# Optimization experiments

Measured on AMD Instinct MI355X. Metric: run time of the kernel, lower is better.

The kernel has to match this reference:

```python
import jax, jax.numpy as jnp
import numpy as np

NUM_HEADS = 4
D_K = 64
D_MODEL = NUM_HEADS * D_K  # 256
SEN_LEN = 8192
N_GROUPS = 4096
BASE_LEN = 64
N_EDGES = N_GROUPS * BASE_LEN  # 262144
PATH_LEN = 64


def setup_inputs() -> dict:
    rng = np.random.default_rng(0)
    key = jax.random.key(0)
    ks = jax.random.split(key, 16)

    # ragged group lengths, each >= 2, summing exactly to N_EDGES
    half = N_GROUPS // 2
    r = rng.integers(-(BASE_LEN - 2), BASE_LEN - 1, size=half)
    edge_len = np.concatenate([BASE_LEN + r, BASE_LEN - r]).astype(np.int64)
    assert edge_len.sum() == N_EDGES and edge_len.min() >= 2

    # distinct token ids; include src=0 and tar=1 so path_agg branches fire
    perm = rng.permutation(np.arange(2, SEN_LEN))[: N_GROUPS - 2]
    token_ids = np.concatenate([np.array([0, 1]), perm]).astype(np.int64)

    def w(k, shape):
        return jax.random.normal(k, shape, jnp.float32) / np.sqrt(shape[-1]).astype(np.float32)

    return {
        "path": jax.random.normal(ks[0], (PATH_LEN, D_MODEL), jnp.float32),
        "path_len": PATH_LEN,
        "q": jax.random.normal(ks[1], (SEN_LEN, D_MODEL), jnp.float32),
        "k": jax.random.normal(ks[2], (N_EDGES, D_MODEL), jnp.float32),
        "v": jax.random.normal(ks[3], (N_EDGES, D_MODEL), jnp.float32),
        "graphs": 0,
        "edge_len": jnp.asarray(edge_len),
        "token_ids": jnp.asarray(token_ids),
        "pair": jnp.array([0, 1], jnp.int32),
        "rev": 0,
        "W_qpair": w(ks[4], (D_MODEL, 2 * D_MODEL)),
        "W_pk": w(ks[5], (D_MODEL, D_MODEL)),
        "W_pv": w(ks[6], (D_MODEL, D_MODEL)),
        "W_q": w(ks[7], (D_MODEL, D_MODEL)),
        "W_k": w(ks[8], (D_MODEL, D_MODEL)),
        "W_v": w(ks[9], (D_MODEL, D_MODEL)),
        "W_out": w(ks[10], (D_MODEL, D_MODEL)),
        "b_out": jnp.zeros((D_MODEL,), jnp.float32),
        "W_agg": w(ks[11], (D_MODEL, 2 * D_MODEL)),
    }


def _forward(path, q, k, v, edge_len, token_ids, pair, rev,
             W_qpair, W_pk, W_pv, W_q, W_k, W_v, W_out, b_out, W_agg):
    H, dk = NUM_HEADS, D_K
    G = edge_len.shape[0]
    E = k.shape[0]
    scale = 1.0 / jnp.sqrt(jnp.float32(dk))

    src = pair[0] if rev == 0 else pair[1]
    tar = pair[1] if rev == 0 else pair[0]

    # pair query: cat(q[src], q[tar]) -> linear -> [H, 1, dk]
    pair_q = (jnp.concatenate([q[src], q[tar]]) @ W_qpair.T).reshape(1, H, dk).transpose(1, 0, 2)

    qh = (q @ W_q.T).reshape(-1, H, dk).transpose(1, 0, 2)      # [H, S, dk]
    pk = (path @ W_pk.T).reshape(-1, H, dk).transpose(1, 0, 2)  # [H, P, dk]
    pv = (path @ W_pv.T).reshape(-1, H, dk).transpose(1, 0, 2)  # [H, P, dk]
    kh = (k @ W_k.T).reshape(-1, H, dk).transpose(1, 0, 2)      # [H, E, dk]
    vh = (v @ W_v.T).reshape(-1, H, dk).transpose(1, 0, 2)      # [H, E, dk]

    # ---- pair/path attention ----
    att = jax.nn.softmax(jnp.einsum('hqd,hpd->hqp', pair_q, pk) * scale, axis=-1)  # [H,1,P]
    path_vals = jnp.einsum('hqp,hpd->hqd', att, pv).sum(axis=1)  # [H, dk]
    path_result = path_vals.reshape(-1) @ W_out.T + b_out        # [d_model]

    # ---- segmented per-group attention (vectorized ragged loop) ----
    seg = jnp.repeat(jnp.arange(G), edge_len, total_repeat_length=E)  # [E]
    q_sel = qh[:, token_ids, :]          # [H, G, dk] query per group
    qe = q_sel[:, seg, :]                # [H, E, dk] query per edge
    # torch.matmul(q_[H,dk], k_[H,i,dk].T) broadcasts to cross-head logits [a,b,i]
    logits = jnp.einsum('aed,bed->eab', qe, kh) * scale  # [E, H, H]
    lmax = jax.lax.stop_gradient(jax.ops.segment_max(logits, seg, num_segments=G))
    ex = jnp.exp(logits - lmax[seg])
    denom = jax.ops.segment_sum(ex, seg, num_segments=G)
    p = ex / denom[seg]                                   # segmented softmax [E, H, H]
    # sum over key-head b per edge, then segment-reduce over edges of each group
    out_e = jnp.einsum('eab,bed->ead', p, vh)             # [E, H, dk]
    hid = jax.ops.segment_sum(out_e, seg, num_segments=G) # [G, H, dk]
    new_hid = hid.reshape(G, H * dk) @ W_out.T + b_out    # [G, d_model] (dropout=identity)

    # ---- assemble output rows ----
    pr = jnp.broadcast_to(path_result, (G, D_MODEL))
    feat_path = jnp.concatenate([new_hid, pr], axis=1) @ W_agg.T  # token == src
    path_feat = jnp.concatenate([pr, new_hid], axis=1) @ W_agg.T  # token == tar
    is_src = (token_ids == src)[:, None]
    is_tar = (token_ids == tar)[:, None]
    vals = jnp.where(is_src, feat_path, jnp.where(is_tar, path_feat, new_hid))
    returned = q.at[token_ids].set(vals)
    return returned, att


def reference(path, path_len, q, k, v, graphs, edge_len, token_ids, pair, rev,
              W_qpair, W_pk, W_pv, W_q, W_k, W_v, W_out, b_out, W_agg):
    return _forward(path, q, k, v, edge_len, token_ids, pair, rev,
                    W_qpair, W_pk, W_pv, W_q, W_k, W_v, W_out, b_out, W_agg)
```

## Files before the change

### kernel.cpp

```cpp
#include <hip/hip_runtime.h>
#include <hip/hip_bf16.h>

#define H 4
#define DK 64
#define DM 256
#define SEN 8192
#define NG 4096
#define ETOT 262144
#define PLEN 64
#define MAXE 128

typedef unsigned short ushortT;
typedef __attribute__((ext_vector_type(8))) __bf16 bf16x8;
typedef __attribute__((ext_vector_type(8))) unsigned short us8;
typedef __attribute__((ext_vector_type(4))) unsigned short us4;
typedef __attribute__((ext_vector_type(4))) float f32x4;

#define TMS 264

__device__ __forceinline__ ushortT f2bf(float f) {
    unsigned u = __float_as_uint(f);
    u += 0x7FFF + ((u >> 16) & 1);
    return (ushortT)(u >> 16);
}
__device__ __forceinline__ bf16x8 ldb8(const ushortT* p) {
    us8 v = *(const us8*)p;
    return __builtin_bit_cast(bf16x8, v);
}
__device__ __forceinline__ bf16x8 pack8(const float* f) {
    us8 v;
#pragma unroll
    for (int j = 0; j < 8; j++) v[j] = f2bf(f[j]);
    return __builtin_bit_cast(bf16x8, v);
}
__device__ __forceinline__ ushortT sbf(float f) {
    return __builtin_bit_cast(ushortT, (__bf16)f);
}
__device__ __forceinline__ bf16x8 pack8f(float4 a, float4 b) {
    bf16x8 r;
    r[0] = (__bf16)a.x; r[1] = (__bf16)a.y; r[2] = (__bf16)a.z; r[3] = (__bf16)a.w;
    r[4] = (__bf16)b.x; r[5] = (__bf16)b.y; r[6] = (__bf16)b.z; r[7] = (__bf16)b.w;
    return r;
}

__global__ __launch_bounds__(256) void scan_kernel(const int* __restrict__ edge_len,
                                                   int* __restrict__ starts) {
    __shared__ int part[256];
    const int tid = threadIdx.x;
    const int base = tid * 16;
    int loc[16];
    int s = 0;
#pragma unroll
    for (int i = 0; i < 16; i++) { loc[i] = s; s += edge_len[base + i]; }
    part[tid] = s;
    __syncthreads();
    if (tid == 0) {
        int acc = 0;
        for (int i = 0; i < 256; i++) { int t = part[i]; part[i] = acc; acc += t; }
    }
    __syncthreads();
    const int off = part[tid];
#pragma unroll
    for (int i = 0; i < 16; i++) starts[base + i] = off + loc[i];
}

__global__ void copy_kernel(const float* __restrict__ q, float* __restrict__ out) {
    const size_t i = (size_t)blockIdx.x * blockDim.x + threadIdx.x;
    ((float4*)out)[i] = ((const float4*)q)[i];
}

__global__ __launch_bounds__(256) void wprep_kernel(
    const float* __restrict__ W_q, const float* __restrict__ W_k,
    const float* __restrict__ W_v, const float* __restrict__ W_out,
    ushortT* __restrict__ WQb, ushortT* __restrict__ WKTb,
    ushortT* __restrict__ WVb, ushortT* __restrict__ WOb) {
    const int idx = blockIdx.x * 256 + threadIdx.x;
    const int sel = idx >> 16;
    const int i = idx & 65535;
    if (sel == 0) {
        WQb[i] = sbf(W_q[i]);
    } else if (sel == 1) {
        const int c = i >> 8, d = i & 255;
        WKTb[i] = sbf(W_k[d * DM + c]);
    } else if (sel == 2) {
        WVb[i] = sbf(W_v[i]);
    } else {
        WOb[i] = sbf(W_out[i]);
    }
}

__global__ __launch_bounds__(256) void qhtmat_kernel(
    const float* __restrict__ q, const int* __restrict__ token_ids,
    const ushortT* __restrict__ WQb, const ushortT* __restrict__ WKTb,
    ushortT* __restrict__ tmat_u) {
    __shared__ ushortT Al[16 * 264];
    __shared__ ushortT QHs[16 * 264];
    const int tid = threadIdx.x;
    const int g0 = blockIdx.x * 16;
    const int lane = tid & 63, w = tid >> 6, lq = lane & 15, lh = lane >> 4;
    {
        const int m = tid >> 4;
        const int c0 = (tid & 15) * 16;
        const int tok = token_ids[g0 + m];
        const float* qr = &q[(size_t)tok * DM + c0];
#pragma unroll
        for (int i = 0; i < 4; i++) {
            float4 v4 = *(const float4*)&qr[i * 4];
            us4 o;
            o[0] = sbf(v4.x); o[1] = sbf(v4.y); o[2] = sbf(v4.z); o[3] = sbf(v4.w);
            *(us4*)&Al[m * 264 + c0 + i * 4] = o;
        }
    }
    __syncthreads();
    {
        bf16x8 af[8];
#pragma unroll
        for (int kk = 0; kk < 8; kk++) af[kk] = ldb8(&Al[lq * 264 + kk * 32 + lh * 8]);
#pragma unroll
        for (int ntl = 0; ntl < 4; ntl++) {
            const int nt = w * 4 + ntl;
            f32x4 acc = {0.f, 0.f, 0.f, 0.f};
#pragma unroll
            for (int kk = 0; kk < 8; kk++) {
                bf16x8 bf = ldb8(&WQb[(nt * 16 + lq) * 256 + kk * 32 + lh * 8]);
                acc = __builtin_amdgcn_mfma_f32_16x16x32_bf16(af[kk], bf, acc, 0, 0, 0);
            }
#pragma unroll
            for (int r = 0; r < 4; r++)
                QHs[(lh * 4 + r) * 264 + nt * 16 + lq] = sbf(acc[r]);
        }
    }
    __syncthreads();
    for (int ab = 0; ab < 16; ab++) {
        const int a = ab >> 2, b = ab & 3;
        bf16x8 a0 = ldb8(&QHs[lq * 264 + a * 64 + lh * 8]);
        bf16x8 a1 = ldb8(&QHs[lq * 264 + a * 64 + 32 + lh * 8]);
#pragma unroll
        for (int ntl = 0; ntl < 4; ntl++) {
            const int nt = w * 4 + ntl;
            f32x4 acc = {0.f, 0.f, 0.f, 0.f};
            bf16x8 b0 = ldb8(&WKTb[(nt * 16 + lq) * 256 + b * 64 + lh * 8]);
            acc = __builtin_amdgcn_mfma_f32_16x16x32_bf16(a0, b0, acc, 0, 0, 0);
            bf16x8 b1 = ldb8(&WKTb[(nt * 16 + lq) * 256 + b * 64 + 32 + lh * 8]);
            acc = __builtin_amdgcn_mfma_f32_16x16x32_bf16(a1, b1, acc, 0, 0, 0);
#pragma unroll
            for (int r = 0; r < 4; r++)
                tmat_u[((size_t)(g0 + lh * 4 + r) * 16 + ab) * 256 + nt * 16 + lq] =
                    sbf(acc[r]);
        }
    }
}

__global__ __launch_bounds__(256) void edge_kernel(
    const float* __restrict__ k, const float* __restrict__ v,
    const int* __restrict__ edge_len, const int* __restrict__ starts,
    ushortT* __restrict__ tmat_u) {
    const int g = blockIdx.x;
    const int tid = threadIdx.x;
    const float scale = 0.125f;
    __shared__ float plog[128][17];
    __shared__ ushortT pT[16 * 136];
    __shared__ float red[16][16];
    __shared__ float mx[16];
    __shared__ float vbuf[32 * 258];
    const int start = starts[g];
    const int len = edge_len[g];
    const int lane = tid & 63, w = tid >> 6, lq = lane & 15, lh = lane >> 4;
    const int rg = tid >> 4, cc = tid & 15;
    const int vrow = tid & 31, vcs = tid >> 5;
    const int nkc = (len + 31) >> 5;

    float4 vr[8];
    {
        const int ecl = (vrow < len) ? vrow : (len - 1);
        const float* src = &v[(size_t)(start + ecl) * DM + vcs * 32];
#pragma unroll
        for (int i = 0; i < 8; i++) vr[i] = *(const float4*)&src[i * 4];
    }

    bf16x8 btm[8];
#pragma unroll
    for (int cb = 0; cb < 8; cb++)
        btm[cb] = ldb8(&tmat_u[((size_t)g * 16 + lq) * 256 + cb * 32 + lh * 8]);

    const int nmt = (len + 15) >> 4;
    for (int t = w; t < nmt; t += 4) {
        const int e = t * 16 + lq;
        const int ec = (e < len) ? e : (len - 1);
        const float* krow = &k[(size_t)(start + ec) * DM + lh * 8];
        f32x4 acc = {0.f, 0.f, 0.f, 0.f};
#pragma unroll
        for (int cb = 0; cb < 8; cb++) {
            float4 k0 = *(const float4*)&krow[cb * 32];
            float4 k1 = *(const float4*)&krow[cb * 32 + 4];
            acc = __builtin_amdgcn_mfma_f32_16x16x32_bf16(pack8f(k0, k1), btm[cb], acc, 0, 0, 0);
        }
#pragma unroll
        for (int r = 0; r < 4; r++) plog[t * 16 + lh * 4 + r][lq] = acc[r] * scale;
    }
    __syncthreads();

    {
        float m = -3.0e38f;
        for (int e = rg; e < len; e += 16) m = fmaxf(m, plog[e][cc]);
        red[rg][cc] = m;
        __syncthreads();
        if (tid < 16) {
            float mm = red[0][tid];
            for (int i2 = 1; i2 < 16; i2++) mm = fmaxf(mm, red[i2][tid]);
            mx[tid] = mm;
        }
        __syncthreads();
        const float mm = mx[cc];
        float s = 0.f;
        for (int e = rg; e < len; e += 16) {
            float ex = __expf(plog[e][cc] - mm);
            plog[e][cc] = ex;
            s += ex;
        }
        red[rg][cc] = s;
        __syncthreads();
        if (tid < 16) {
            float ss = red[0][tid];
            for (int i2 = 1; i2 < 16; i2++) ss += red[i2][tid];
            mx[tid] = 1.0f / ss;
        }
        __syncthreads();
        const float inv = mx[cc];
        const int padlen = nkc * 32;
        for (int e = rg; e < padlen; e += 16) {
            float pv = (e < len) ? plog[e][cc] * inv : 0.f;
            pT[cc * 136 + e] = f2bf(pv);
        }
    }
    __syncthreads();

    {
        f32x4 uacc[4];
#pragma unroll
        for (int nt = 0; nt < 4; nt++) uacc[nt] = {0.f, 0.f, 0.f, 0.f};
        const int wb = vrow * 258 + vcs * 32;
        for (int kc = 0; kc < nkc; kc++) {
#pragma unroll
            for (int i = 0; i < 8; i++) {
                *(float2*)&vbuf[wb + i * 4]     = make_float2(vr[i].x, vr[i].y);
                *(float2*)&vbuf[wb + i * 4 + 2] = make_float2(vr[i].z, vr[i].w);
            }
            __syncthreads();
            if (kc + 1 < nkc) {
                const int e = (kc + 1) * 32 + vrow;
                const int ecl = (e < len) ? e : (len - 1);
                const float* src = &v[(size_t)(start + ecl) * DM + vcs * 32];
#pragma unroll
                for (int i = 0; i < 8; i++) vr[i] = *(const float4*)&src[i * 4];
            }
            bf16x8 ap = ldb8(&pT[lq * 136 + kc * 32 + lh * 8]);
#pragma unroll
            for (int nt = 0; nt < 4; nt++) {
                bf16x8 bv;
#pragma unroll
                for (int j = 0; j < 8; j++)
                    bv[j] = (__bf16)vbuf[(lh * 8 + j) * 258 + w * 64 + nt * 16 + lq];
                uacc[nt] = __builtin_amdgcn_mfma_f32_16x16x32_bf16(ap, bv, uacc[nt], 0, 0, 0);
            }
            __syncthreads();
        }
        const int c0 = w * 64;
#pragma unroll
        for (int nt = 0; nt < 4; nt++) {
#pragma unroll
            for (int r = 0; r < 4; r++) {
                const int ab = lh * 4 + r;
                tmat_u[((size_t)g * 16 + ab) * 256 + c0 + nt * 16 + lq] = sbf(uacc[nt][r]);
            }
        }
    }
}

__global__ __launch_bounds__(256) void hidnh_kernel(
    const ushortT* __restrict__ Ub, const ushortT* __restrict__ WVb,
    const ushortT* __restrict__ WOb, const float* __restrict__ b_out,
    const int* __restrict__ token_ids, float* __restrict__ out) {
    __shared__ ushortT HIDs[16 * 264];
    const int tid = threadIdx.x;
    const int g0 = blockIdx.x * 16;
    const int lane = tid & 63, w = tid >> 6, lq = lane & 15, lh = lane >> 4;
#pragma unroll
    for (int a = 0; a < 4; a++) {
        f32x4 acc = {0.f, 0.f, 0.f, 0.f};
        for (int kk = 0; kk < 32; kk++) {
            const int kbase = kk * 32 + lh * 8;
            bf16x8 af = ldb8(&Ub[((size_t)(g0 + lq) * 16 + a * 4) * 256 + kbase]);
            bf16x8 bf = ldb8(&WVb[(size_t)((kbase >> 8) * 64 + w * 16 + lq) * 256 + (kbase & 255)]);
            acc = __builtin_amdgcn_mfma_f32_16x16x32_bf16(af, bf, acc, 0, 0, 0);
        }
#pragma unroll
        for (int r = 0; r < 4; r++)
            HIDs[(lh * 4 + r) * 264 + a * 64 + w * 16 + lq] = sbf(acc[r]);
    }
    __syncthreads();
    bf16x8 af2[8];
#pragma unroll
    for (int kk = 0; kk < 8; kk++) af2[kk] = ldb8(&HIDs[lq * 264 + kk * 32 + lh * 8]);
    int toks[4];
#pragma unroll
    for (int r = 0; r < 4; r++) toks[r] = token_ids[g0 + lh * 4 + r];
#pragma unroll
    for (int ntl = 0; ntl < 4; ntl++) {
        const int nt = w * 4 + ntl;
        f32x4 acc = {0.f, 0.f, 0.f, 0.f};
#pragma unroll
        for (int kk = 0; kk < 8; kk++) {
            bf16x8 bf = ldb8(&WOb[(nt * 16 + lq) * 256 + kk * 32 + lh * 8]);
            acc = __builtin_amdgcn_mfma_f32_16x16x32_bf16(af2[kk], bf, acc, 0, 0, 0);
        }
        const int n = nt * 16 + lq;
        const float bo = b_out[n];
#pragma unroll
        for (int r = 0; r < 4; r++)
            out[(size_t)toks[r] * DM + n] = acc[r] + bo;
    }
}

__global__ __launch_bounds__(256) void agg_kernel(
    const int* __restrict__ token_ids, const int* __restrict__ pair,
    const int* __restrict__ rev, const float* __restrict__ W_agg,
    const float* __restrict__ path_result, float* __restrict__ out) {
    __shared__ int gsrc, gtar;
    __shared__ float catS[512], catT[512];
    const int tid = threadIdx.x;
    if (tid == 0) { gsrc = -1; gtar = -1; }
    __syncthreads();
    const int rv = rev[0];
    const int src = (rv == 0) ? pair[0] : pair[1];
    const int tar = (rv == 0) ? pair[1] : pair[0];
    for (int i = tid; i < NG; i += 256) {
        const int tk = token_ids[i];
        if (tk == src) gsrc = i;
        if (tk == tar) gtar = i;
    }
    __syncthreads();
    const int gs = gsrc, gt = gtar;
    if (gs >= 0) {
        catS[tid] = out[(size_t)src * DM + tid];
        catS[256 + tid] = path_result[tid];
    }
    if (gt >= 0) {
        catT[tid] = path_result[tid];
        catT[256 + tid] = out[(size_t)tar * DM + tid];
    }
    __syncthreads();
    if (gs >= 0) {
        float acc = 0.f;
        for (int n = 0; n < 512; n += 4) {
            float4 w4 = *(const float4*)&W_agg[(size_t)tid * 512 + n];
            acc += w4.x * catS[n] + w4.y * catS[n + 1] + w4.z * catS[n + 2] + w4.w * catS[n + 3];
        }
        out[(size_t)src * DM + tid] = acc;
    }
    if (gt >= 0) {
        float acc = 0.f;
        for (int n = 0; n < 512; n += 4) {
            float4 w4 = *(const float4*)&W_agg[(size_t)tid * 512 + n];
            acc += w4.x * catT[n] + w4.y * catT[n + 1] + w4.z * catT[n + 2] + w4.w * catT[n + 3];
        }
        out[(size_t)tar * DM + tid] = acc;
    }
}

__global__ __launch_bounds__(256) void pathB_kernel(
    const float* __restrict__ path, const float* __restrict__ q,
    const int* __restrict__ pair, const int* __restrict__ rev,
    const float* __restrict__ W_qpair, const float* __restrict__ W_pk,
    const float* __restrict__ W_pv,
    float* __restrict__ pv_ws, float* __restrict__ logits_ws) {
    __shared__ float cat[512];
    __shared__ float pq[256];
    __shared__ float prow[256];
    __shared__ float lp[256];
    const int p = blockIdx.x;
    const int tid = threadIdx.x;
    const int rv = rev[0];
    const int src = (rv == 0) ? pair[0] : pair[1];
    const int tar = (rv == 0) ? pair[1] : pair[0];
    cat[tid] = q[(size_t)src * DM + tid];
    cat[256 + tid] = q[(size_t)tar * DM + tid];
    prow[tid] = path[p * DM + tid];
    __syncthreads();
    float acc = 0.f;
    for (int c = 0; c < 512; c += 4) {
        float4 w4 = *(const float4*)&W_qpair[(size_t)tid * 512 + c];
        acc += w4.x * cat[c] + w4.y * cat[c + 1] + w4.z * cat[c + 2] + w4.w * cat[c + 3];
    }
    pq[tid] = acc;
    __syncthreads();
    float pkv = 0.f, pvv = 0.f;
    for (int c = 0; c < 256; c += 4) {
        float4 a4 = *(const float4*)&W_pk[tid * DM + c];
        float4 b4 = *(const float4*)&W_pv[tid * DM + c];
        float4 x4 = *(const float4*)&prow[c];
        pkv += a4.x * x4.x + a4.y * x4.y + a4.z * x4.z + a4.w * x4.w;
        pvv += b4.x * x4.x + b4.y * x4.y + b4.z * x4.z + b4.w * x4.w;
    }
    pv_ws[p * DM + tid] = pvv;
    lp[tid] = pq[tid] * pkv;
    __syncthreads();
    if (tid < H) {
        float s = 0.f;
        for (int d = 0; d < DK; d++) s += lp[tid * DK + d];
        logits_ws[tid * PLEN + p] = s * 0.125f;
    }
}

__global__ __launch_bounds__(256) void pathC_kernel(
    const float* __restrict__ pv_ws, const float* __restrict__ logits_ws,
    const float* __restrict__ W_out, const float* __restrict__ b_out,
    float* __restrict__ att_out, float* __restrict__ path_result) {
    __shared__ float att[256];
    __shared__ float pvals[256];
    const int tid = threadIdx.x;
    att[tid] = logits_ws[tid];
    __syncthreads();
    if (tid < H) {
        float m = -3.0e38f;
        for (int p = 0; p < PLEN; p++) m = fmaxf(m, att[tid * PLEN + p]);
        float s = 0.f;
        for (int p = 0; p < PLEN; p++) {
            float e = __expf(att[tid * PLEN + p] - m);
            att[tid * PLEN + p] = e;
            s += e;
        }
        float inv = 1.f / s;
        for (int p = 0; p < PLEN; p++) att[tid * PLEN + p] *= inv;
    }
    __syncthreads();
    att_out[tid] = att[tid];
    {
        const int h = tid >> 6;
        float a = 0.f;
        for (int p = 0; p < PLEN; p++) a += att[h * PLEN + p] * pv_ws[p * DM + tid];
        pvals[tid] = a;
    }
    __syncthreads();
    {
        float a = b_out[tid];
        for (int c = 0; c < 256; c += 4) {
            float4 w4 = *(const float4*)&W_out[tid * DM + c];
            a += w4.x * pvals[c] + w4.y * pvals[c + 1] + w4.z * pvals[c + 2] + w4.w * pvals[c + 3];
        }
        path_result[tid] = a;
    }
}

__global__ __launch_bounds__(256, 4) void group_kernel(
    const float* __restrict__ q, const float* __restrict__ k, const float* __restrict__ v,
    const int* __restrict__ edge_len, const int* __restrict__ token_ids,
    const int* __restrict__ pair, const int* __restrict__ rev,
    const float* __restrict__ W_q,
    const float* __restrict__ W_k, const float* __restrict__ W_v,
    const float* __restrict__ W_out, const float* __restrict__ b_out,
    const float* __restrict__ W_agg,
    const int* __restrict__ starts, const float* __restrict__ path_result,
    float* __restrict__ out) {
    const int g = blockIdx.x;
    const int tid = threadIdx.x;
    const float scale = 0.125f;

    __shared__ float qrow[256];
    __shared__ float qh[256];
    __shared__ ushortT qh_b[4 * 72];
    __shared__ ushortT tmat_b[16 * TMS];
    __shared__ float plog[128][17];
    __shared__ ushortT pT[16 * 136];
    __shared__ ushortT u_b[4 * 1032];
    __shared__ float hid[256];
    __shared__ float nh[256];
    __shared__ float red[16][16];
    __shared__ float mx[16];

    const int tok = token_ids[g];
    const int start = starts[g];
    const int len = edge_len[g];

    const int lane = tid & 63;
    const int w = tid >> 6;
    const int lq = lane & 15;
    const int lh = lane >> 4;
    const int rg = tid >> 4;
    const int cc = tid & 15;

    qrow[tid] = q[(size_t)tok * DM + tid];
    __syncthreads();

    for (int i = 0; i < 16; i++) {
        const int r = i * 16 + rg;
        float acc = 0.f;
#pragma unroll
        for (int j4 = 0; j4 < 4; j4++) {
            const int c0 = j4 * 64 + cc * 4;
            float4 w4 = *(const float4*)&W_q[r * DM + c0];
            float4 x4 = *(const float4*)&qrow[c0];
            acc += w4.x * x4.x + w4.y * x4.y + w4.z * x4.z + w4.w * x4.w;
        }
#pragma unroll
        for (int off = 8; off; off >>= 1) acc += __shfl_down(acc, off, 16);
        if (cc == 0) qh[r] = acc;
    }
    __syncthreads();
    qh_b[(tid >> 6) * 72 + (tid & 63)] = f2bf(qh[tid]);
    __syncthreads();

    {
        const int arow = (lq < 3) ? lq : 3;
        bf16x8 aq0 = ldb8(&qh_b[arow * 72 + lh * 8]);
        bf16x8 aq1 = ldb8(&qh_b[arow * 72 + 32 + lh * 8]);
        for (int nt = 0; nt < 16; nt++) {
            const int c = nt * 16 + lq;
            f32x4 acc = {0.f, 0.f, 0.f, 0.f};
            float wf[8];
#pragma unroll
            for (int j = 0; j < 8; j++)
                wf[j] = W_k[(size_t)(w * 64 + lh * 8 + j) * DM + c];
            acc = __builtin_amdgcn_mfma_f32_16x16x32_bf16(aq0, pack8(wf), acc, 0, 0, 0);
#pragma unroll
            for (int j = 0; j < 8; j++)
                wf[j] = W_k[(size_t)(w * 64 + 32 + lh * 8 + j) * DM + c];
            acc = __builtin_amdgcn_mfma_f32_16x16x32_bf16(aq1, pack8(wf), acc, 0, 0, 0);
            if (lane < 16) {
#pragma unroll
                for (int r = 0; r < 4; r++)
                    tmat_b[(r * 4 + w) * TMS + nt * 16 + lq] = f2bf(acc[r]);
            }
        }
    }
    __syncthreads();

    {
        bf16x8 btm[8];
#pragma unroll
        for (int cb = 0; cb < 8; cb++)
            btm[cb] = ldb8(&tmat_b[lq * TMS + cb * 32 + lh * 8]);
        const int nmt = (len + 15) >> 4;
        for (int t = w; t < nmt; t += 4) {
            const int e = t * 16 + lq;
            const int ec = (e < len) ? e : (len - 1);
            const float* krow = &k[(size_t)(start + ec) * DM + lh * 8];
            f32x4 acc = {0.f, 0.f, 0.f, 0.f};
#pragma unroll
            for (int cb = 0; cb < 8; cb++) {
                float4 k0 = *(const float4*)&krow[cb * 32];
                float4 k1 = *(const float4*)&krow[cb * 32 + 4];
                float kf[8] = {k0.x, k0.y, k0.z, k0.w, k1.x, k1.y, k1.z, k1.w};
                acc = __builtin_amdgcn_mfma_f32_16x16x32_bf16(pack8(kf), btm[cb], acc, 0, 0, 0);
            }
#pragma unroll
            for (int r = 0; r < 4; r++) plog[t * 16 + lh * 4 + r][lq] = acc[r] * scale;
        }
    }
    __syncthreads();

    const int nkc = (len + 31) >> 5;
    {
        float m = -3.0e38f;
        for (int e = rg; e < len; e += 16) m = fmaxf(m, plog[e][cc]);
        red[rg][cc] = m;
        __syncthreads();
        if (tid < 16) {
            float mm = red[0][tid];
            for (int i2 = 1; i2 < 16; i2++) mm = fmaxf(mm, red[i2][tid]);
            mx[tid] = mm;
        }
        __syncthreads();
        const float mm = mx[cc];
        float s = 0.f;
        for (int e = rg; e < len; e += 16) {
            float ex = __expf(plog[e][cc] - mm);
            plog[e][cc] = ex;
            s += ex;
        }
        red[rg][cc] = s;
        __syncthreads();
        if (tid < 16) {
            float ss = red[0][tid];
            for (int i2 = 1; i2 < 16; i2++) ss += red[i2][tid];
            mx[tid] = 1.0f / ss;
        }
        __syncthreads();
        const float inv = mx[cc];
        const int padlen = nkc * 32;
        for (int e = rg; e < padlen; e += 16) {
            float pv = (e < len) ? plog[e][cc] * inv : 0.f;
            pT[cc * 136 + e] = f2bf(pv);
        }
    }
    __syncthreads();

    {
        f32x4 uacc[4];
#pragma unroll
        for (int nt = 0; nt < 4; nt++) uacc[nt] = {0.f, 0.f, 0.f, 0.f};
        const int c0 = w * 64;
#pragma unroll
        for (int kc = 0; kc < 4; kc++) {
            if (kc < nkc) {
                bf16x8 ap = ldb8(&pT[lq * 136 + kc * 32 + lh * 8]);
#pragma unroll
                for (int nt = 0; nt < 4; nt++) {
                    float bf[8];
#pragma unroll
                    for (int j = 0; j < 8; j++) {
                        int e = kc * 32 + lh * 8 + j;
                        int ecl = (e < len) ? e : (len - 1);
                        bf[j] = v[(size_t)(start + ecl) * DM + c0 + nt * 16 + lq];
                    }
                    uacc[nt] = __builtin_amdgcn_mfma_f32_16x16x32_bf16(ap, pack8(bf), uacc[nt], 0, 0, 0);
                }
            }
        }
#pragma unroll
        for (int nt = 0; nt < 4; nt++) {
#pragma unroll
            for (int r = 0; r < 4; r++) {
                const int row = lh * 4 + r;
                const int a = row >> 2, b = row & 3;
                u_b[a * 1032 + b * 256 + c0 + nt * 16 + lq] = f2bf(uacc[nt][r]);
            }
        }
    }
    __syncthreads();

    {
        const int arow = (lq < 3) ? lq : 3;
        f32x4 hacc = {0.f, 0.f, 0.f, 0.f};
        for (int kc = 0; kc < 32; kc++) {
            bf16x8 au = ldb8(&u_b[arow * 1032 + kc * 32 + lh * 8]);
            const int kk = kc * 32 + lh * 8;
            const float* wr = &W_v[(size_t)((kk >> 8) * 64 + w * 16 + lq) * DM + (kk & 255)];
            float4 w0 = *(const float4*)&wr[0];
            float4 w1 = *(const float4*)&wr[4];
            float wf[8] = {w0.x, w0.y, w0.z, w0.w, w1.x, w1.y, w1.z, w1.w};
            hacc = __builtin_amdgcn_mfma_f32_16x16x32_bf16(au, pack8(wf), hacc, 0, 0, 0);
        }
        if (lane < 16) {
#pragma unroll
            for (int r = 0; r < 4; r++) hid[r * 64 + w * 16 + lq] = hacc[r];
        }
    }
    __syncthreads();

    for (int i = 0; i < 16; i++) {
        const int m = i * 16 + rg;
        float acc = 0.f;
#pragma unroll
        for (int j4 = 0; j4 < 4; j4++) {
            const int c0 = j4 * 64 + cc * 4;
            float4 w4 = *(const float4*)&W_out[m * DM + c0];
            float4 h4 = *(const float4*)&hid[c0];
            acc += w4.x * h4.x + w4.y * h4.y + w4.z * h4.z + w4.w * h4.w;
        }
#pragma unroll
        for (int off = 8; off; off >>= 1) acc += __shfl_down(acc, off, 16);
        if (cc == 0) nh[m] = b_out[m] + acc;
    }
    __syncthreads();

    const int rv = rev[0];
    const int src = (rv == 0) ? pair[0] : pair[1];
    const int tar = (rv == 0) ? pair[1] : pair[0];
    float val;
    if (tok == src || tok == tar) {
        qrow[tid] = path_result[tid];
        __syncthreads();
        const float* x1 = (tok == src) ? nh : qrow;
        const float* x2 = (tok == src) ? qrow : nh;
        float acc = 0.f;
        for (int n = 0; n < 256; n += 4) {
            float4 w4 = *(const float4*)&W_agg[(size_t)tid * 512 + n];
            acc += w4.x * x1[n] + w4.y * x1[n + 1] + w4.z * x1[n + 2] + w4.w * x1[n + 3];
        }
        for (int n = 0; n < 256; n += 4) {
            float4 w4 = *(const float4*)&W_agg[(size_t)tid * 512 + 256 + n];
            acc += w4.x * x2[n] + w4.y * x2[n + 1] + w4.z * x2[n + 2] + w4.w * x2[n + 3];
        }
        val = acc;
    } else {
        val = nh[tid];
    }
    out[(size_t)tok * DM + tid] = val;
}

extern "C" void kernel_launch(void* const* d_in, const int* in_sizes, int n_in,
                              void* d_out, int out_size, void* d_ws, size_t ws_size,
                              hipStream_t stream) {
    const float* path    = (const float*)d_in[0];
    const float* q       = (const float*)d_in[2];
    const float* k       = (const float*)d_in[3];
    const float* v       = (const float*)d_in[4];
    const int*   edge_len  = (const int*)d_in[6];
    const int*   token_ids = (const int*)d_in[7];
    const int*   pair      = (const int*)d_in[8];
    const int*   rev       = (const int*)d_in[9];
    const float* W_qpair = (const float*)d_in[10];
    const float* W_pk    = (const float*)d_in[11];
    const float* W_pv    = (const float*)d_in[12];
    const float* W_q     = (const float*)d_in[13];
    const float* W_k     = (const float*)d_in[14];
    const float* W_v     = (const float*)d_in[15];
    const float* W_out   = (const float*)d_in[16];
    const float* b_out   = (const float*)d_in[17];
    const float* W_agg   = (const float*)d_in[18];
    float* out = (float*)d_out;

    char* base = (char*)d_ws;
    int*    starts      = (int*)(base + 0);
    float*  path_result = (float*)(base + 16384);
    float*  pv_ws       = (float*)(base + 17408);
    float*  logits_ws   = (float*)(base + 82944);
    ushortT* WQb        = (ushortT*)(base + 83968);
    ushortT* WKTb       = (ushortT*)(base + 215040);
    ushortT* WVb        = (ushortT*)(base + 346112);
    ushortT* WOb        = (ushortT*)(base + 477184);
    ushortT* tmat_u     = (ushortT*)(base + 608256);
    const size_t NEED = 608256 + 33554432;

    copy_kernel<<<dim3(2048), dim3(256), 0, stream>>>(q, out);
    scan_kernel<<<dim3(1), dim3(256), 0, stream>>>(edge_len, starts);
    pathB_kernel<<<dim3(PLEN), dim3(256), 0, stream>>>(path, q, pair, rev, W_qpair, W_pk,
                                                       W_pv, pv_ws, logits_ws);
    pathC_kernel<<<dim3(1), dim3(256), 0, stream>>>(pv_ws, logits_ws, W_out, b_out,
                                                    out + (size_t)SEN * DM, path_result);

    if (ws_size >= NEED) {
        wprep_kernel<<<dim3(1024), dim3(256), 0, stream>>>(W_q, W_k, W_v, W_out,
                                                           WQb, WKTb, WVb, WOb);
        qhtmat_kernel<<<dim3(256), dim3(256), 0, stream>>>(q, token_ids, WQb, WKTb, tmat_u);
        edge_kernel<<<dim3(NG), dim3(256), 0, stream>>>(k, v, edge_len, starts, tmat_u);
        hidnh_kernel<<<dim3(256), dim3(256), 0, stream>>>(tmat_u, WVb, WOb, b_out,
                                                          token_ids, out);
        agg_kernel<<<dim3(1), dim3(256), 0, stream>>>(token_ids, pair, rev, W_agg,
                                                      path_result, out);
    } else {
        group_kernel<<<dim3(NG), dim3(256), 0, stream>>>(q, k, v, edge_len, token_ids, pair,
                                                         rev, W_q, W_k, W_v, W_out, b_out,
                                                         W_agg, starts, path_result, out);
    }
}
```

Measured before the change: 300.8 us.

## Halve groups per block in qhtmat/hidnh, bf16 V staging, occupancy hint on edge kernel

qhtmat and hidnh now handle 8 groups per block instead of 16 and launch twice as many blocks. Their 16-row MFMA tiles duplicate rows and only half the lanes write results, which trades wasted MFMA work for more parallelism across CUs. The edge kernel stages V in shared memory as bf16 instead of fp32, cutting LDS footprint and conversion work in the inner loop. It also adds a launch_bounds minimum of 5 blocks per CU and uses the hardware bf16 conversion for probabilities, which may raise register pressure.

```diff
diff --git a/kernel.cpp b/kernel.cpp
--- a/kernel.cpp
+++ b/kernel.cpp
@@ -17,6 +17,7 @@
 typedef __attribute__((ext_vector_type(4))) float f32x4;
 
 #define TMS 264
+#define VBS 260
 
 __device__ __forceinline__ ushortT f2bf(float f) {
     unsigned u = __float_as_uint(f);
@@ -35,6 +36,9 @@
 }
 __device__ __forceinline__ ushortT sbf(float f) {
     return __builtin_bit_cast(ushortT, (__bf16)f);
+}
+__device__ __forceinline__ __bf16 u2b(ushortT u) {
+    return __builtin_bit_cast(__bf16, u);
 }
 __device__ __forceinline__ bf16x8 pack8f(float4 a, float4 b) {
     bf16x8 r;
@@ -93,29 +97,30 @@
     const float* __restrict__ q, const int* __restrict__ token_ids,
     const ushortT* __restrict__ WQb, const ushortT* __restrict__ WKTb,
     ushortT* __restrict__ tmat_u) {
-    __shared__ ushortT Al[16 * 264];
-    __shared__ ushortT QHs[16 * 264];
+    __shared__ ushortT Al[8 * 264];
+    __shared__ ushortT QHs[8 * 264];
     const int tid = threadIdx.x;
-    const int g0 = blockIdx.x * 16;
+    const int g0 = blockIdx.x * 8;
     const int lane = tid & 63, w = tid >> 6, lq = lane & 15, lh = lane >> 4;
     {
-        const int m = tid >> 4;
-        const int c0 = (tid & 15) * 16;
+        const int m = tid >> 5;
+        const int c0 = (tid & 31) * 8;
         const int tok = token_ids[g0 + m];
         const float* qr = &q[(size_t)tok * DM + c0];
-#pragma unroll
-        for (int i = 0; i < 4; i++) {
-            float4 v4 = *(const float4*)&qr[i * 4];
-            us4 o;
-            o[0] = sbf(v4.x); o[1] = sbf(v4.y); o[2] = sbf(v4.z); o[3] = sbf(v4.w);
-            *(us4*)&Al[m * 264 + c0 + i * 4] = o;
-        }
-    }
-    __syncthreads();
-    {
+        float4 v0 = *(const float4*)&qr[0];
+        float4 v1 = *(const float4*)&qr[4];
+        us4 o0, o1;
+        o0[0] = sbf(v0.x); o0[1] = sbf(v0.y); o0[2] = sbf(v0.z); o0[3] = sbf(v0.w);
+        o1[0] = sbf(v1.x); o1[1] = sbf(v1.y); o1[2] = sbf(v1.z); o1[3] = sbf(v1.w);
+        *(us4*)&Al[m * 264 + c0] = o0;
+        *(us4*)&Al[m * 264 + c0 + 4] = o1;
+    }
+    __syncthreads();
+    {
+        const int arow = lq & 7;
         bf16x8 af[8];
 #pragma unroll
-        for (int kk = 0; kk < 8; kk++) af[kk] = ldb8(&Al[lq * 264 + kk * 32 + lh * 8]);
+        for (int kk = 0; kk < 8; kk++) af[kk] = ldb8(&Al[arow * 264 + kk * 32 + lh * 8]);
 #pragma unroll
         for (int ntl = 0; ntl < 4; ntl++) {
             const int nt = w * 4 + ntl;
@@ -125,16 +130,19 @@
                 bf16x8 bf = ldb8(&WQb[(nt * 16 + lq) * 256 + kk * 32 + lh * 8]);
                 acc = __builtin_amdgcn_mfma_f32_16x16x32_bf16(af[kk], bf, acc, 0, 0, 0);
             }
-#pragma unroll
-            for (int r = 0; r < 4; r++)
-                QHs[(lh * 4 + r) * 264 + nt * 16 + lq] = sbf(acc[r]);
+            if (lh < 2) {
+#pragma unroll
+                for (int r = 0; r < 4; r++)
+                    QHs[(lh * 4 + r) * 264 + nt * 16 + lq] = sbf(acc[r]);
+            }
         }
     }
     __syncthreads();
     for (int ab = 0; ab < 16; ab++) {
         const int a = ab >> 2, b = ab & 3;
-        bf16x8 a0 = ldb8(&QHs[lq * 264 + a * 64 + lh * 8]);
-        bf16x8 a1 = ldb8(&QHs[lq * 264 + a * 64 + 32 + lh * 8]);
+        const int arow = lq & 7;
+        bf16x8 a0 = ldb8(&QHs[arow * 264 + a * 64 + lh * 8]);
+        bf16x8 a1 = ldb8(&QHs[arow * 264 + a * 64 + 32 + lh * 8]);
 #pragma unroll
         for (int ntl = 0; ntl < 4; ntl++) {
             const int nt = w * 4 + ntl;
@@ -143,15 +151,17 @@
             acc = __builtin_amdgcn_mfma_f32_16x16x32_bf16(a0, b0, acc, 0, 0, 0);
             bf16x8 b1 = ldb8(&WKTb[(nt * 16 + lq) * 256 + b * 64 + 32 + lh * 8]);
             acc = __builtin_amdgcn_mfma_f32_16x16x32_bf16(a1, b1, acc, 0, 0, 0);
-#pragma unroll
-            for (int r = 0; r < 4; r++)
-                tmat_u[((size_t)(g0 + lh * 4 + r) * 16 + ab) * 256 + nt * 16 + lq] =
-                    sbf(acc[r]);
-        }
-    }
-}
-
-__global__ __launch_bounds__(256) void edge_kernel(
+            if (lh < 2) {
+#pragma unroll
+                for (int r = 0; r < 4; r++)
+                    tmat_u[((size_t)(g0 + lh * 4 + r) * 16 + ab) * 256 + nt * 16 + lq] =
+                        sbf(acc[r]);
+            }
+        }
+    }
+}
+
+__global__ __launch_bounds__(256, 5) void edge_kernel(
     const float* __restrict__ k, const float* __restrict__ v,
     const int* __restrict__ edge_len, const int* __restrict__ starts,
     ushortT* __restrict__ tmat_u) {
@@ -162,7 +172,7 @@
     __shared__ ushortT pT[16 * 136];
     __shared__ float red[16][16];
     __shared__ float mx[16];
-    __shared__ float vbuf[32 * 258];
+    __shared__ ushortT vbuf[32 * VBS];
     const int start = starts[g];
     const int len = edge_len[g];
     const int lane = tid & 63, w = tid >> 6, lq = lane & 15, lh = lane >> 4;
@@ -230,7 +240,7 @@
         const int padlen = nkc * 32;
         for (int e = rg; e < padlen; e += 16) {
             float pv = (e < len) ? plog[e][cc] * inv : 0.f;
-            pT[cc * 136 + e] = f2bf(pv);
+            pT[cc * 136 + e] = sbf(pv);
         }
     }
     __syncthreads();
@@ -239,12 +249,14 @@
         f32x4 uacc[4];
 #pragma unroll
         for (int nt = 0; nt < 4; nt++) uacc[nt] = {0.f, 0.f, 0.f, 0.f};
-        const int wb = vrow * 258 + vcs * 32;
+        const int wb = vrow * VBS + vcs * 32;
         for (int kc = 0; kc < nkc; kc++) {
 #pragma unroll
             for (int i = 0; i < 8; i++) {
-                *(float2*)&vbuf[wb + i * 4]     = make_float2(vr[i].x, vr[i].y);
-                *(float2*)&vbuf[wb + i * 4 + 2] = make_float2(vr[i].z, vr[i].w);
+                us4 o;
+                o[0] = sbf(vr[i].x); o[1] = sbf(vr[i].y);
+                o[2] = sbf(vr[i].z); o[3] = sbf(vr[i].w);
+                *(us4*)&vbuf[wb + i * 4] = o;
             }
             __syncthreads();
             if (kc + 1 < nkc) {
@@ -260,7 +272,7 @@
                 bf16x8 bv;
 #pragma unroll
                 for (int j = 0; j < 8; j++)
-                    bv[j] = (__bf16)vbuf[(lh * 8 + j) * 258 + w * 64 + nt * 16 + lq];
+                    bv[j] = u2b(vbuf[(lh * 8 + j) * VBS + w * 64 + nt * 16 + lq]);
                 uacc[nt] = __builtin_amdgcn_mfma_f32_16x16x32_bf16(ap, bv, uacc[nt], 0, 0, 0);
             }
             __syncthreads();
@@ -281,30 +293,36 @@
     const ushortT* __restrict__ Ub, const ushortT* __restrict__ WVb,
     const ushortT* __restrict__ WOb, const float* __restrict__ b_out,
     const int* __restrict__ token_ids, float* __restrict__ out) {
-    __shared__ ushortT HIDs[16 * 264];
+    __shared__ ushortT HIDs[8 * 264];
     const int tid = threadIdx.x;
-    const int g0 = blockIdx.x * 16;
+    const int g0 = blockIdx.x * 8;
     const int lane = tid & 63, w = tid >> 6, lq = lane & 15, lh = lane >> 4;
+    const int grow = g0 + (lq & 7);
 #pragma unroll
     for (int a = 0; a < 4; a++) {
         f32x4 acc = {0.f, 0.f, 0.f, 0.f};
         for (int kk = 0; kk < 32; kk++) {
             const int kbase = kk * 32 + lh * 8;
-            bf16x8 af = ldb8(&Ub[((size_t)(g0 + lq) * 16 + a * 4) * 256 + kbase]);
+            bf16x8 af = ldb8(&Ub[((size_t)grow * 16 + a * 4) * 256 + kbase]);
             bf16x8 bf = ldb8(&WVb[(size_t)((kbase >> 8) * 64 + w * 16 + lq) * 256 + (kbase & 255)]);
             acc = __builtin_amdgcn_mfma_f32_16x16x32_bf16(af, bf, acc, 0, 0, 0);
         }
-#pragma unroll
-        for (int r = 0; r < 4; r++)
-            HIDs[(lh * 4 + r) * 264 + a * 64 + w * 16 + lq] = sbf(acc[r]);
+        if (lh < 2) {
+#pragma unroll
+            for (int r = 0; r < 4; r++)
+                HIDs[(lh * 4 + r) * 264 + a * 64 + w * 16 + lq] = sbf(acc[r]);
+        }
     }
     __syncthreads();
     bf16x8 af2[8];
 #pragma unroll
-    for (int kk = 0; kk < 8; kk++) af2[kk] = ldb8(&HIDs[lq * 264 + kk * 32 + lh * 8]);
+    for (int kk = 0; kk < 8; kk++) af2[kk] = ldb8(&HIDs[(lq & 7) * 264 + kk * 32 + lh * 8]);
     int toks[4];
 #pragma unroll
-    for (int r = 0; r < 4; r++) toks[r] = token_ids[g0 + lh * 4 + r];
+    for (int r = 0; r < 4; r++) {
+        int gi = g0 + lh * 4 + r;
+        toks[r] = token_ids[(gi < NG) ? gi : (NG - 1)];
+    }
 #pragma unroll
     for (int ntl = 0; ntl < 4; ntl++) {
         const int nt = w * 4 + ntl;
@@ -316,9 +334,11 @@
         }
         const int n = nt * 16 + lq;
         const float bo = b_out[n];
-#pragma unroll
-        for (int r = 0; r < 4; r++)
-            out[(size_t)toks[r] * DM + n] = acc[r] + bo;
+        if (lh < 2) {
+#pragma unroll
+            for (int r = 0; r < 4; r++)
+                out[(size_t)toks[r] * DM + n] = acc[r] + bo;
+        }
     }
 }
 
@@ -733,9 +753,9 @@
     if (ws_size >= NEED) {
         wprep_kernel<<<dim3(1024), dim3(256), 0, stream>>>(W_q, W_k, W_v, W_out,
                                                            WQb, WKTb, WVb, WOb);
-        qhtmat_kernel<<<dim3(256), dim3(256), 0, stream>>>(q, token_ids, WQb, WKTb, tmat_u);
+        qhtmat_kernel<<<dim3(512), dim3(256), 0, stream>>>(q, token_ids, WQb, WKTb, tmat_u);
         edge_kernel<<<dim3(NG), dim3(256), 0, stream>>>(k, v, edge_len, starts, tmat_u);
-        hidnh_kernel<<<dim3(256), dim3(256), 0, stream>>>(tmat_u, WVb, WOb, b_out,
+        hidnh_kernel<<<dim3(512), dim3(256), 0, stream>>>(tmat_u, WVb, WOb, b_out,
                                                           token_ids, out);
         agg_kernel<<<dim3(1), dim3(256), 0, stream>>>(token_ids, pair, rev, W_agg,
                                                       path_result, out);
```

Result: slower. 348.2 us (+15.7%).

## Assign one wavefront per group in edge kernel with register-resident softmax

Applied to the files above, without the earlier changes.

Reworks the edge attention kernel so each 64-lane wavefront handles a whole group, four groups per block, instead of one group per 256-thread block. Logits stay in registers and the softmax max/sum reductions use cross-lane shuffles, which removes the shared-memory logit buffer and most block-wide barriers. V rows are converted to bf16 once when staged into a per-wave LDS tile, and each wave accumulates all 16 output column tiles itself. The trade-off is much higher register pressure (16 accumulators plus 32 logit values), load imbalance across the ragged group lengths inside a block, and no prefetching of V.

```diff
diff --git a/kernel.cpp b/kernel.cpp
--- a/kernel.cpp
+++ b/kernel.cpp
@@ -14,6 +14,7 @@
 typedef __attribute__((ext_vector_type(8))) __bf16 bf16x8;
 typedef __attribute__((ext_vector_type(8))) unsigned short us8;
 typedef __attribute__((ext_vector_type(4))) unsigned short us4;
+typedef __attribute__((ext_vector_type(2))) unsigned short us2;
 typedef __attribute__((ext_vector_type(4))) float f32x4;
 
 #define TMS 264
@@ -35,6 +36,9 @@
 }
 __device__ __forceinline__ ushortT sbf(float f) {
     return __builtin_bit_cast(ushortT, (__bf16)f);
+}
+__device__ __forceinline__ __bf16 u2b(ushortT u) {
+    return __builtin_bit_cast(__bf16, u);
 }
 __device__ __forceinline__ bf16x8 pack8f(float4 a, float4 b) {
     bf16x8 r;
@@ -151,129 +155,135 @@
     }
 }
 
-__global__ __launch_bounds__(256) void edge_kernel(
+__global__ __launch_bounds__(256, 3) void edge_kernel(
     const float* __restrict__ k, const float* __restrict__ v,
     const int* __restrict__ edge_len, const int* __restrict__ starts,
     ushortT* __restrict__ tmat_u) {
-    const int g = blockIdx.x;
     const int tid = threadIdx.x;
-    const float scale = 0.125f;
-    __shared__ float plog[128][17];
-    __shared__ ushortT pT[16 * 136];
-    __shared__ float red[16][16];
-    __shared__ float mx[16];
-    __shared__ float vbuf[32 * 258];
+    const int w = tid >> 6, lane = tid & 63;
+    const int lq = lane & 15, lh = lane >> 4;
+    const int g = blockIdx.x * 4 + w;
+    __shared__ ushortT pTs[4][16 * 136];
+    __shared__ ushortT vbs[4][32 * 134];
+    ushortT* pT = pTs[w];
+    ushortT* vb = vbs[w];
     const int start = starts[g];
     const int len = edge_len[g];
-    const int lane = tid & 63, w = tid >> 6, lq = lane & 15, lh = lane >> 4;
-    const int rg = tid >> 4, cc = tid & 15;
-    const int vrow = tid & 31, vcs = tid >> 5;
+    const int nmt = (len + 15) >> 4;
     const int nkc = (len + 31) >> 5;
-
-    float4 vr[8];
-    {
-        const int ecl = (vrow < len) ? vrow : (len - 1);
-        const float* src = &v[(size_t)(start + ecl) * DM + vcs * 32];
-#pragma unroll
-        for (int i = 0; i < 8; i++) vr[i] = *(const float4*)&src[i * 4];
-    }
+    const float scale = 0.125f;
 
     bf16x8 btm[8];
 #pragma unroll
     for (int cb = 0; cb < 8; cb++)
         btm[cb] = ldb8(&tmat_u[((size_t)g * 16 + lq) * 256 + cb * 32 + lh * 8]);
 
-    const int nmt = (len + 15) >> 4;
-    for (int t = w; t < nmt; t += 4) {
-        const int e = t * 16 + lq;
-        const int ec = (e < len) ? e : (len - 1);
-        const float* krow = &k[(size_t)(start + ec) * DM + lh * 8];
-        f32x4 acc = {0.f, 0.f, 0.f, 0.f};
-#pragma unroll
-        for (int cb = 0; cb < 8; cb++) {
-            float4 k0 = *(const float4*)&krow[cb * 32];
-            float4 k1 = *(const float4*)&krow[cb * 32 + 4];
-            acc = __builtin_amdgcn_mfma_f32_16x16x32_bf16(pack8f(k0, k1), btm[cb], acc, 0, 0, 0);
-        }
-#pragma unroll
-        for (int r = 0; r < 4; r++) plog[t * 16 + lh * 4 + r][lq] = acc[r] * scale;
-    }
-    __syncthreads();
-
-    {
-        float m = -3.0e38f;
-        for (int e = rg; e < len; e += 16) m = fmaxf(m, plog[e][cc]);
-        red[rg][cc] = m;
-        __syncthreads();
-        if (tid < 16) {
-            float mm = red[0][tid];
-            for (int i2 = 1; i2 < 16; i2++) mm = fmaxf(mm, red[i2][tid]);
-            mx[tid] = mm;
-        }
-        __syncthreads();
-        const float mm = mx[cc];
-        float s = 0.f;
-        for (int e = rg; e < len; e += 16) {
-            float ex = __expf(plog[e][cc] - mm);
-            plog[e][cc] = ex;
-            s += ex;
-        }
-        red[rg][cc] = s;
-        __syncthreads();
-        if (tid < 16) {
-            float ss = red[0][tid];
-            for (int i2 = 1; i2 < 16; i2++) ss += red[i2][tid];
-            mx[tid] = 1.0f / ss;
-        }
-        __syncthreads();
-        const float inv = mx[cc];
-        const int padlen = nkc * 32;
-        for (int e = rg; e < padlen; e += 16) {
-            float pv = (e < len) ? plog[e][cc] * inv : 0.f;
-            pT[cc * 136 + e] = f2bf(pv);
-        }
-    }
-    __syncthreads();
-
-    {
-        f32x4 uacc[4];
-#pragma unroll
-        for (int nt = 0; nt < 4; nt++) uacc[nt] = {0.f, 0.f, 0.f, 0.f};
-        const int wb = vrow * 258 + vcs * 32;
-        for (int kc = 0; kc < nkc; kc++) {
-#pragma unroll
-            for (int i = 0; i < 8; i++) {
-                *(float2*)&vbuf[wb + i * 4]     = make_float2(vr[i].x, vr[i].y);
-                *(float2*)&vbuf[wb + i * 4 + 2] = make_float2(vr[i].z, vr[i].w);
-            }
-            __syncthreads();
-            if (kc + 1 < nkc) {
-                const int e = (kc + 1) * 32 + vrow;
-                const int ecl = (e < len) ? e : (len - 1);
-                const float* src = &v[(size_t)(start + ecl) * DM + vcs * 32];
-#pragma unroll
-                for (int i = 0; i < 8; i++) vr[i] = *(const float4*)&src[i * 4];
-            }
-            bf16x8 ap = ldb8(&pT[lq * 136 + kc * 32 + lh * 8]);
-#pragma unroll
-            for (int nt = 0; nt < 4; nt++) {
-                bf16x8 bv;
-#pragma unroll
-                for (int j = 0; j < 8; j++)
-                    bv[j] = (__bf16)vbuf[(lh * 8 + j) * 258 + w * 64 + nt * 16 + lq];
-                uacc[nt] = __builtin_amdgcn_mfma_f32_16x16x32_bf16(ap, bv, uacc[nt], 0, 0, 0);
-            }
-            __syncthreads();
-        }
-        const int c0 = w * 64;
-#pragma unroll
-        for (int nt = 0; nt < 4; nt++) {
+    float pv[8][4];
+#pragma unroll
+    for (int t = 0; t < 8; t++) {
+        if (t < nmt) {
+            const int e = t * 16 + lq;
+            const int ec = (e < len) ? e : (len - 1);
+            const float* krow = &k[(size_t)(start + ec) * DM + lh * 8];
+            f32x4 acc = {0.f, 0.f, 0.f, 0.f};
+#pragma unroll
+            for (int cb = 0; cb < 8; cb++) {
+                float4 k0 = *(const float4*)&krow[cb * 32];
+                float4 k1 = *(const float4*)&krow[cb * 32 + 4];
+                acc = __builtin_amdgcn_mfma_f32_16x16x32_bf16(pack8f(k0, k1), btm[cb], acc, 0, 0, 0);
+            }
+#pragma unroll
+            for (int r = 0; r < 4; r++) pv[t][r] = acc[r] * scale;
+        }
+    }
+
+    float mxv = -3.0e38f;
+#pragma unroll
+    for (int t = 0; t < 8; t++) {
+        if (t < nmt) {
 #pragma unroll
             for (int r = 0; r < 4; r++) {
-                const int ab = lh * 4 + r;
-                tmat_u[((size_t)g * 16 + ab) * 256 + c0 + nt * 16 + lq] = sbf(uacc[nt][r]);
-            }
-        }
+                const int e = t * 16 + lh * 4 + r;
+                if (e < len) mxv = fmaxf(mxv, pv[t][r]);
+                else pv[t][r] = -3.0e38f;
+            }
+        }
+    }
+    mxv = fmaxf(mxv, __shfl_xor(mxv, 16));
+    mxv = fmaxf(mxv, __shfl_xor(mxv, 32));
+    float sum = 0.f;
+#pragma unroll
+    for (int t = 0; t < 8; t++) {
+        if (t < nmt) {
+#pragma unroll
+            for (int r = 0; r < 4; r++) {
+                float ex = __expf(pv[t][r] - mxv);
+                pv[t][r] = ex;
+                sum += ex;
+            }
+        }
+    }
+    sum += __shfl_xor(sum, 16);
+    sum += __shfl_xor(sum, 32);
+    const float inv = 1.0f / sum;
+
+    const int npt = nkc * 2;
+#pragma unroll
+    for (int t = 0; t < 8; t++) {
+        if (t < npt) {
+            us2 o0, o1;
+            if (t < nmt) {
+                o0[0] = sbf(pv[t][0] * inv); o0[1] = sbf(pv[t][1] * inv);
+                o1[0] = sbf(pv[t][2] * inv); o1[1] = sbf(pv[t][3] * inv);
+            } else {
+                o0[0] = 0; o0[1] = 0; o1[0] = 0; o1[1] = 0;
+            }
+            *(us2*)&pT[lq * 136 + t * 16 + lh * 4] = o0;
+            *(us2*)&pT[lq * 136 + t * 16 + lh * 4 + 2] = o1;
+        }
+    }
+
+    f32x4 uacc[16];
+#pragma unroll
+    for (int nt = 0; nt < 16; nt++) uacc[nt] = {0.f, 0.f, 0.f, 0.f};
+    const int srow = lane & 31, sseg = lane >> 5;
+#pragma unroll
+    for (int ch = 0; ch < 4; ch++) {
+        if (ch < nkc) {
+            bf16x8 ap = ldb8(&pT[lq * 136 + ch * 32 + lh * 8]);
+#pragma unroll
+            for (int half = 0; half < 2; half++) {
+                {
+                    const int e = ch * 32 + srow;
+                    const int ecl = (e < len) ? e : (len - 1);
+                    const float* vr = &v[(size_t)(start + ecl) * DM + half * 128 + sseg * 64];
+#pragma unroll
+                    for (int i = 0; i < 8; i++) {
+                        float4 a = *(const float4*)&vr[i * 8];
+                        float4 b = *(const float4*)&vr[i * 8 + 4];
+                        us8 o;
+                        o[0] = sbf(a.x); o[1] = sbf(a.y); o[2] = sbf(a.z); o[3] = sbf(a.w);
+                        o[4] = sbf(b.x); o[5] = sbf(b.y); o[6] = sbf(b.z); o[7] = sbf(b.w);
+                        *(us8*)&vb[srow * 134 + sseg * 64 + i * 8] = o;
+                    }
+                }
+#pragma unroll
+                for (int ntl = 0; ntl < 8; ntl++) {
+                    const int nt = half * 8 + ntl;
+                    bf16x8 bv;
+#pragma unroll
+                    for (int j = 0; j < 8; j++)
+                        bv[j] = u2b(vb[(lh * 8 + j) * 134 + ntl * 16 + lq]);
+                    uacc[nt] = __builtin_amdgcn_mfma_f32_16x16x32_bf16(ap, bv, uacc[nt], 0, 0, 0);
+                }
+            }
+        }
+    }
+#pragma unroll
+    for (int nt = 0; nt < 16; nt++) {
+#pragma unroll
+        for (int r = 0; r < 4; r++)
+            tmat_u[((size_t)g * 16 + lh * 4 + r) * 256 + nt * 16 + lq] = sbf(uacc[nt][r]);
     }
 }
 
@@ -734,7 +744,7 @@
         wprep_kernel<<<dim3(1024), dim3(256), 0, stream>>>(W_q, W_k, W_v, W_out,
                                                            WQb, WKTb, WVb, WOb);
         qhtmat_kernel<<<dim3(256), dim3(256), 0, stream>>>(q, token_ids, WQb, WKTb, tmat_u);
-        edge_kernel<<<dim3(NG), dim3(256), 0, stream>>>(k, v, edge_len, starts, tmat_u);
+        edge_kernel<<<dim3(1024), dim3(256), 0, stream>>>(k, v, edge_len, starts, tmat_u);
         hidnh_kernel<<<dim3(256), dim3(256), 0, stream>>>(tmat_u, WVb, WOb, b_out,
                                                           token_ids, out);
         agg_kernel<<<dim3(1), dim3(256), 0, stream>>>(token_ids, pair, rev, W_agg,
```

New measurement: 320.3 us. 1.06x slower.

## Split edge kernel into softmax-logits kernel and one-wave-per-group PV kernel

Applied to the files above, without the earlier changes.

The fused per-group edge kernel is split in two. The first kernel computes the logits and the segmented softmax, then writes the normalized probabilities as bf16 into the tmat_u workspace. A second kernel assigns one wavefront per group and reads V straight from global memory into MFMA operands, with no LDS staging and no block barriers. The aim is to remove LDS traffic and synchronisation from the PV step and to let more groups run in parallel. The cost is an extra launch, a round trip of the probabilities through global memory, and poorly vectorized strided scalar loads of V.

```diff
diff --git a/kernel.cpp b/kernel.cpp
--- a/kernel.cpp
+++ b/kernel.cpp
@@ -151,32 +151,20 @@
     }
 }
 
-__global__ __launch_bounds__(256) void edge_kernel(
-    const float* __restrict__ k, const float* __restrict__ v,
+__global__ __launch_bounds__(256) void logitsm_kernel(
+    const float* __restrict__ k,
     const int* __restrict__ edge_len, const int* __restrict__ starts,
     ushortT* __restrict__ tmat_u) {
     const int g = blockIdx.x;
     const int tid = threadIdx.x;
     const float scale = 0.125f;
     __shared__ float plog[128][17];
-    __shared__ ushortT pT[16 * 136];
     __shared__ float red[16][16];
     __shared__ float mx[16];
-    __shared__ float vbuf[32 * 258];
     const int start = starts[g];
     const int len = edge_len[g];
     const int lane = tid & 63, w = tid >> 6, lq = lane & 15, lh = lane >> 4;
     const int rg = tid >> 4, cc = tid & 15;
-    const int vrow = tid & 31, vcs = tid >> 5;
-    const int nkc = (len + 31) >> 5;
-
-    float4 vr[8];
-    {
-        const int ecl = (vrow < len) ? vrow : (len - 1);
-        const float* src = &v[(size_t)(start + ecl) * DM + vcs * 32];
-#pragma unroll
-        for (int i = 0; i < 8; i++) vr[i] = *(const float4*)&src[i * 4];
-    }
 
     bf16x8 btm[8];
 #pragma unroll
@@ -227,53 +215,60 @@
         }
         __syncthreads();
         const float inv = mx[cc];
-        const int padlen = nkc * 32;
-        for (int e = rg; e < padlen; e += 16) {
-            float pv = (e < len) ? plog[e][cc] * inv : 0.f;
-            pT[cc * 136 + e] = f2bf(pv);
-        }
-    }
-    __syncthreads();
-
-    {
-        f32x4 uacc[4];
-#pragma unroll
-        for (int nt = 0; nt < 4; nt++) uacc[nt] = {0.f, 0.f, 0.f, 0.f};
-        const int wb = vrow * 258 + vcs * 32;
-        for (int kc = 0; kc < nkc; kc++) {
-#pragma unroll
-            for (int i = 0; i < 8; i++) {
-                *(float2*)&vbuf[wb + i * 4]     = make_float2(vr[i].x, vr[i].y);
-                *(float2*)&vbuf[wb + i * 4 + 2] = make_float2(vr[i].z, vr[i].w);
+        const int e0 = rg * 8;
+        us8 o;
+#pragma unroll
+        for (int j = 0; j < 8; j++) {
+            const int e = e0 + j;
+            const float p = (e < len) ? plog[e][cc] * inv : 0.f;
+            o[j] = sbf(p);
+        }
+        *(us8*)&tmat_u[((size_t)g * 16 + cc) * 256 + e0] = o;
+    }
+}
+
+__global__ __launch_bounds__(256) void pv_kernel(
+    const float* __restrict__ v,
+    const int* __restrict__ edge_len, const int* __restrict__ starts,
+    ushortT* __restrict__ tmat_u) {
+    const int tid = threadIdx.x;
+    const int w = tid >> 6, lane = tid & 63;
+    const int lq = lane & 15, lh = lane >> 4;
+    const int g = blockIdx.x * 4 + w;
+    const int start = starts[g];
+    const int len = edge_len[g];
+    const int nkc = (len + 31) >> 5;
+
+    bf16x8 ap[4];
+#pragma unroll
+    for (int kc = 0; kc < 4; kc++)
+        ap[kc] = ldb8(&tmat_u[((size_t)g * 16 + lq) * 256 + kc * 32 + lh * 8]);
+
+    f32x4 uacc[16];
+#pragma unroll
+    for (int nt = 0; nt < 16; nt++) uacc[nt] = {0.f, 0.f, 0.f, 0.f};
+
+#pragma unroll
+    for (int kc = 0; kc < 4; kc++) {
+        if (kc < nkc) {
+#pragma unroll
+            for (int nt = 0; nt < 16; nt++) {
+                bf16x8 bv;
+#pragma unroll
+                for (int j = 0; j < 8; j++) {
+                    const int e = kc * 32 + lh * 8 + j;
+                    const int ecl = (e < len) ? e : (len - 1);
+                    bv[j] = (__bf16)v[(size_t)(start + ecl) * DM + nt * 16 + lq];
+                }
+                uacc[nt] = __builtin_amdgcn_mfma_f32_16x16x32_bf16(ap[kc], bv, uacc[nt], 0, 0, 0);
             }
-            __syncthreads();
-            if (kc + 1 < nkc) {
-                const int e = (kc + 1) * 32 + vrow;
-                const int ecl = (e < len) ? e : (len - 1);
-                const float* src = &v[(size_t)(start + ecl) * DM + vcs * 32];
-#pragma unroll
-                for (int i = 0; i < 8; i++) vr[i] = *(const float4*)&src[i * 4];
-            }
-            bf16x8 ap = ldb8(&pT[lq * 136 + kc * 32 + lh * 8]);
-#pragma unroll
-            for (int nt = 0; nt < 4; nt++) {
-                bf16x8 bv;
-#pragma unroll
-                for (int j = 0; j < 8; j++)
-                    bv[j] = (__bf16)vbuf[(lh * 8 + j) * 258 + w * 64 + nt * 16 + lq];
-                uacc[nt] = __builtin_amdgcn_mfma_f32_16x16x32_bf16(ap, bv, uacc[nt], 0, 0, 0);
-            }
-            __syncthreads();
-        }
-        const int c0 = w * 64;
-#pragma unroll
-        for (int nt = 0; nt < 4; nt++) {
-#pragma unroll
-            for (int r = 0; r < 4; r++) {
-                const int ab = lh * 4 + r;
-                tmat_u[((size_t)g * 16 + ab) * 256 + c0 + nt * 16 + lq] = sbf(uacc[nt][r]);
-            }
-        }
+        }
+    }
+#pragma unroll
+    for (int nt = 0; nt < 16; nt++) {
+#pragma unroll
+        for (int r = 0; r < 4; r++)
+            tmat_u[((size_t)g * 16 + lh * 4 + r) * 256 + nt * 16 + lq] = sbf(uacc[nt][r]);
     }
 }
 
@@ -734,7 +729,8 @@
         wprep_kernel<<<dim3(1024), dim3(256), 0, stream>>>(W_q, W_k, W_v, W_out,
                                                            WQb, WKTb, WVb, WOb);
         qhtmat_kernel<<<dim3(256), dim3(256), 0, stream>>>(q, token_ids, WQb, WKTb, tmat_u);
-        edge_kernel<<<dim3(NG), dim3(256), 0, stream>>>(k, v, edge_len, starts, tmat_u);
+        logitsm_kernel<<<dim3(NG), dim3(256), 0, stream>>>(k, edge_len, starts, tmat_u);
+        pv_kernel<<<dim3(NG / 4), dim3(256), 0, stream>>>(v, edge_len, starts, tmat_u);
         hidnh_kernel<<<dim3(256), dim3(256), 0, stream>>>(tmat_u, WVb, WOb, b_out,
                                                           token_ids, out);
         agg_kernel<<<dim3(1), dim3(256), 0, stream>>>(token_ids, pair, rev, W_agg,
```

Result: slower. 323.5 us (+7.5%).
